# Optimization experiments

Measured on AMD Instinct MI355X. Metric: run time of the kernel, lower is better.

Reference implementation:

```python
import jax, jax.numpy as jnp
import numpy as np


def setup_inputs() -> dict:
    key = jax.random.key(0)
    k1, k2, k3, k4 = jax.random.split(key, 4)
    B, S, D_IN, D_OUT = 4, 4096, 768, 128
    x = jax.random.normal(k1, (B, S, D_IN), dtype=jnp.float32)
    # torch Linear(d_in, d_out) weight is [d_out, d_in]; we store transposed [d_in, d_out]
    scale = 1.0 / np.sqrt(D_IN)
    Wq = jax.random.normal(k2, (D_IN, D_OUT), dtype=jnp.float32) * scale
    Wk = jax.random.normal(k3, (D_IN, D_OUT), dtype=jnp.float32) * scale
    Wv = jax.random.normal(k4, (D_IN, D_OUT), dtype=jnp.float32) * scale
    return {"x": x, "Wq": Wq, "Wk": Wk, "Wv": Wv}


def reference(x, Wq, Wk, Wv):
    # x: [B, S, d_in]; Wq/Wk/Wv: [d_in, d_out]
    B, S, _ = x.shape
    q = jnp.einsum('bsd,de->bse', x, Wq)
    k = jnp.einsum('bsd,de->bse', x, Wk)
    v = jnp.einsum('bsd,de->bse', x, Wv)
    d_out = k.shape[-1]
    scores = jnp.einsum('bqe,bke->bqk', q, k)  # [B, S, S]
    causal = jnp.tril(jnp.ones((S, S), dtype=bool))  # True where attention allowed
    scores = jnp.where(causal[None], scores, -jnp.inf)
    attn = jax.nn.softmax(scores / jnp.sqrt(jnp.float32(d_out)), axis=-1)
    # dropout prob is 0.0 -> identity
    return jnp.einsum('bqk,bke->bqe', attn, v)
```

## Files before the change

kernel.cpp:

```cpp
#include <hip/hip_runtime.h>
#include <stdint.h>

typedef unsigned short u16;
typedef uint32_t u32;
typedef __bf16 bf16;
typedef bf16 bf16x8 __attribute__((ext_vector_type(8)));
typedef bf16 bf16x4 __attribute__((ext_vector_type(4)));
typedef short s16x4 __attribute__((ext_vector_type(4)));
typedef float f32x4 __attribute__((ext_vector_type(4)));
typedef uint32_t u32x4 __attribute__((ext_vector_type(4)));

#define S_LEN 4096
#define D_IN 768
#define D_OUT 128
#define NB 4
#define M_TOTAL (NB * S_LEN)
#define NPROP 115

__device__ const unsigned char SPLITS_T[16] = {1,2,3,4,4,5,6,7,8,8,9,10,11,12,12,13};
__device__ const unsigned char OFF_T[16]    = {0,1,3,6,10,14,19,25,32,40,48,57,67,78,90,102};
__device__ const unsigned char TILE_OF[NPROP] = {
    0, 1,1, 2,2,2, 3,3,3,3, 4,4,4,4, 5,5,5,5,5, 6,6,6,6,6,6, 7,7,7,7,7,7,7,
    8,8,8,8,8,8,8,8, 9,9,9,9,9,9,9,9, 10,10,10,10,10,10,10,10,10,
    11,11,11,11,11,11,11,11,11,11, 12,12,12,12,12,12,12,12,12,12,12,
    13,13,13,13,13,13,13,13,13,13,13,13, 14,14,14,14,14,14,14,14,14,14,14,14,
    15,15,15,15,15,15,15,15,15,15,15,15,15};

static __device__ __forceinline__ u16 f2bf(float f) {
    union { float f; uint32_t u; } c; c.f = f;
    return (u16)((c.u + 0x7FFFu + ((c.u >> 16) & 1u)) >> 16);
}
static __device__ __forceinline__ float bf2f_lo(uint32_t w) { return __uint_as_float(w << 16); }
static __device__ __forceinline__ float bf2f_hi(uint32_t w) { return __uint_as_float(w & 0xFFFF0000u); }

static __device__ __forceinline__ bf16x8 ld8(const u16* p) {
    union { u32x4 v; bf16x8 b; } c;
    c.v = *reinterpret_cast<const u32x4*>(p);
    return c.b;
}

static __device__ __forceinline__ f32x4 mfma16(bf16x8 a, bf16x8 b, f32x4 c) {
    return __builtin_amdgcn_mfma_f32_16x16x32_bf16(a, b, c, 0, 0, 0);
}

static __device__ __forceinline__ f32x4 mfma16k16(uint2 a, uint2 b, f32x4 c) {
#if defined(__HIP_DEVICE_COMPILE__)
#if __has_builtin(__builtin_amdgcn_mfma_f32_16x16x16_bf16)
    union { uint2 u; bf16x4 v; } ca, cb; ca.u = a; cb.u = b;
    return __builtin_amdgcn_mfma_f32_16x16x16_bf16(ca.v, cb.v, c, 0, 0, 0);
#else
    union { uint2 u; s16x4 v; } ca, cb; ca.u = a; cb.u = b;
    return __builtin_amdgcn_mfma_f32_16x16x16bf16_1k(ca.v, cb.v, c, 0, 0, 0);
#endif
#else
    (void)a; (void)b;
    return c;
#endif
}

static __device__ __forceinline__ void gload16(const void* g, void* l) {
    __builtin_amdgcn_global_load_lds((const __attribute__((address_space(1))) uint32_t*)g,
                                     (__attribute__((address_space(3))) uint32_t*)l, 16, 0, 0);
}

static __device__ __forceinline__ float bpermf(int addr, float v) {
    return __int_as_float(__builtin_amdgcn_ds_bpermute(addr, __float_as_int(v)));
}
static __device__ __forceinline__ u32 pk2(float a, float b) {
    return __builtin_amdgcn_perm(__float_as_uint(b), __float_as_uint(a), 0x07060302u);
}

__global__ __launch_bounds__(256) void wt_kernel(const float* __restrict__ Wq, const float* __restrict__ Wk,
                                                 const float* __restrict__ Wv, u16* __restrict__ Wt) {
    __shared__ u16 tl[128][40];
    const int w = blockIdx.x / 24;
    const int kc = (blockIdx.x % 24) * 32;
    const float* W = (w == 0) ? Wq : (w == 1) ? Wk : Wv;
#pragma unroll
    for (int p = 0; p < 4; ++p) {
        int kr = p * 8 + (threadIdx.x >> 5);
        int nc = (threadIdx.x & 31) * 4;
        float4 v = *reinterpret_cast<const float4*>(W + (size_t)(kc + kr) * D_OUT + nc);
        tl[nc + 0][kr] = f2bf(v.x); tl[nc + 1][kr] = f2bf(v.y);
        tl[nc + 2][kr] = f2bf(v.z); tl[nc + 3][kr] = f2bf(v.w);
    }
    __syncthreads();
    const int n = threadIdx.x >> 1, kh = (threadIdx.x & 1) * 16;
    u32x4* dst = reinterpret_cast<u32x4*>(Wt + (size_t)w * D_OUT * D_IN + (size_t)n * D_IN + kc + kh);
    const u32x4* src = reinterpret_cast<const u32x4*>(&tl[n][kh]);
    dst[0] = src[0];
    dst[1] = src[1];
}

__global__ __launch_bounds__(256) void qkv_kernel(const float* __restrict__ x, const u16* __restrict__ Wt,
                                                  u16* __restrict__ Qb, u16* __restrict__ Kb,
                                                  u16* __restrict__ Vt) {
    __shared__ __align__(16) u16 wslab[2][192 * 32];
    __shared__ __align__(16) float xslab[2][32 * 32];
    const int wave = threadIdx.x >> 6, lane = threadIdx.x & 63;
    const int r = lane & 15, g = lane >> 4;
    const int m0 = blockIdx.x * 32;
    const int h = blockIdx.y;

    f32x4 acc[3][2];
#pragma unroll
    for (int y = 0; y < 3; ++y)
#pragma unroll
        for (int f = 0; f < 2; ++f) acc[y][f] = f32x4{0.f, 0.f, 0.f, 0.f};

    auto stageW = [&](int bb, int kk) {
#pragma unroll
        for (int i = 0; i < 3; ++i) {
            int c = wave * 3 + i;
            int rr = c * 16 + (lane >> 2);
            int gr = (rr >> 6) * 128 + h * 64 + (rr & 63);
            const u16* src = Wt + (size_t)gr * D_IN + kk * 32 + (((lane & 3) ^ (rr & 3)) * 8);
            gload16(src, &wslab[bb][c * 512]);
        }
    };
    auto stageX = [&](int bb, int kk) {
        int c = wave;
        int row = c * 8 + (lane >> 3);
        const float* src = x + (size_t)(m0 + row) * D_IN + kk * 32 + (((lane & 7) ^ (row & 7)) * 4);
        gload16(src, &xslab[bb][c * 256]);
    };

    stageW(0, 0);
    stageX(0, 0);
    int buf = 0;
    const int arow = (wave >> 1) * 16 + r;
    const int ch = (wave & 1) * 32;
    for (int kk = 0; kk < 24; ++kk) {
        int kn = (kk + 1 < 24) ? kk + 1 : 0;
        stageX(buf ^ 1, kn);
        stageW(buf ^ 1, kn);
        asm volatile("s_waitcnt vmcnt(4)" ::: "memory");
        __builtin_amdgcn_sched_barrier(0);
        __builtin_amdgcn_s_barrier();
        f32x4 xa0 = *reinterpret_cast<const f32x4*>(&xslab[buf][arow * 32 + (((2 * g) ^ (arow & 7)) * 4)]);
        f32x4 xa1 = *reinterpret_cast<const f32x4*>(&xslab[buf][arow * 32 + (((2 * g + 1) ^ (arow & 7)) * 4)]);
        union { u16 u[8]; bf16x8 bv; } af;
#pragma unroll
        for (int t = 0; t < 4; ++t) { af.u[t] = f2bf(xa0[t]); af.u[4 + t] = f2bf(xa1[t]); }
#pragma unroll
        for (int y = 0; y < 3; ++y)
#pragma unroll
            for (int f = 0; f < 2; ++f) {
                int rr = y * 64 + ch + f * 16 + r;
                bf16x8 wf = ld8(&wslab[buf][rr * 32 + ((g ^ (r & 3)) * 8)]);
                acc[y][f] = mfma16(af.bv, wf, acc[y][f]);
            }
        __builtin_amdgcn_s_barrier();
        buf ^= 1;
    }
    asm volatile("s_waitcnt vmcnt(0)" ::: "memory");

    const float QSC = 0.1275174366f;
#pragma unroll
    for (int f = 0; f < 2; ++f)
#pragma unroll
        for (int i = 0; i < 4; ++i) {
            int mrow = m0 + (wave >> 1) * 16 + 4 * g + i;
            int col = h * 64 + ch + f * 16 + r;
            Qb[(size_t)mrow * D_OUT + col] = f2bf(acc[0][f][i] * QSC);
            Kb[(size_t)mrow * D_OUT + col] = f2bf(acc[1][f][i]);
            Vt[((size_t)((mrow >> 12) * D_OUT + col)) * S_LEN + (mrow & 4095)] = f2bf(acc[2][f][i]);
        }
}

__global__ __launch_bounds__(512, 2) void attn_kernel(const u16* __restrict__ Qb, const u16* __restrict__ Kb,
                                                      const u16* __restrict__ Vt, u16* __restrict__ Po,
                                                      float* __restrict__ Pml, float* __restrict__ out,
                                                      int mode) {
    __shared__ __align__(16) u16 kbuf[2][64 * 128];
    __shared__ __align__(16) u16 vbuf[2][128 * 64];

    const int wave = threadIdx.x >> 6, lane = threadIdx.x & 63;
    const int r = lane & 15, g = lane >> 4;
    const int n = (int)blockIdx.x;
    int b, t, s, sp;
    if (mode) {
        b = n / NPROP;
        const int idx = n - b * NPROP;
        t = TILE_OF[idx];
        s = idx - OFF_T[t];
        sp = SPLITS_T[t];
    } else {
        b = n >> 4; t = n & 15; s = 0; sp = 1;
    }
    const int nj = 4 * t + 4;
    const int qw0 = t * 256 + wave * 32;

    const u16* Kp = Kb + (size_t)b * S_LEN * D_OUT;
    const u16* Vp = Vt + (size_t)b * D_OUT * S_LEN;

    bf16x8 qf[2][4];
#pragma unroll
    for (int rb = 0; rb < 2; ++rb)
#pragma unroll
        for (int kk = 0; kk < 4; ++kk)
            qf[rb][kk] = ld8(Qb + ((size_t)(b * S_LEN + qw0 + rb * 16 + r)) * D_OUT + kk * 32 + 8 * g);

    f32x4 o[2][8];
    float l_[2];
#pragma unroll
    for (int rb = 0; rb < 2; ++rb) {
#pragma unroll
        for (int f = 0; f < 8; ++f) o[rb][f] = f32x4{0.f, 0.f, 0.f, 0.f};
        l_[rb] = 0.f;
    }

    const int lx16 = (lane ^ 16) * 4, lx32 = (lane ^ 32) * 4;

    auto stageK = [&](int bb, int k0) {
#pragma unroll
        for (int i = 0; i < 2; ++i) {
            int c = i * 8 + wave;
            int row = c * 4 + (lane >> 4);
            const u16* src = Kp + (size_t)(k0 + row) * D_OUT + (((lane & 15) ^ (row & 7)) * 8);
            gload16(src, &kbuf[bb][c * 512]);
        }
    };
    auto stageV = [&](int bb, int k0) {
#pragma unroll
        for (int i = 0; i < 2; ++i) {
            int c = i * 8 + wave;
            int row = c * 8 + (lane >> 3);
            const u16* src = Vp + (size_t)row * S_LEN + k0 + (((lane & 7) ^ (row & 7)) * 8);
            gload16(src, &vbuf[bb][c * 512]);
        }
    };

    stageK(0, s * 64);
    stageV(0, s * 64);
    int buf = 0;
    for (int j = s; j < nj; j += sp) {
        const int k0 = j * 64;
        asm volatile("s_waitcnt vmcnt(0)" ::: "memory");
        __builtin_amdgcn_sched_barrier(0);
        __builtin_amdgcn_s_barrier();
        const int j2 = j + sp;
        if (j2 < nj) {
            stageK(buf ^ 1, j2 * 64);
            stageV(buf ^ 1, j2 * 64);
        }

        f32x4 sv[2][4];
#pragma unroll
        for (int rb = 0; rb < 2; ++rb)
#pragma unroll
            for (int f = 0; f < 4; ++f) sv[rb][f] = f32x4{0.f, 0.f, 0.f, 0.f};
        __builtin_amdgcn_s_setprio(1);
#pragma unroll
        for (int kk = 0; kk < 4; ++kk)
#pragma unroll
            for (int f = 0; f < 4; ++f) {
                bf16x8 kf = ld8(&kbuf[buf][(f * 16 + r) * 128 + (((kk * 4 + g) ^ (r & 7)) * 8)]);
                sv[0][f] = mfma16(kf, qf[0][kk], sv[0][f]);
                sv[1][f] = mfma16(kf, qf[1][kk], sv[1][f]);
            }
        __builtin_amdgcn_s_setprio(0);

        uint2 pb[2][4];
#pragma unroll
        for (int rb = 0; rb < 2; ++rb) {
            const int qrb = qw0 + rb * 16;
            const int q = qrb + r;
            if (k0 + 63 > qrb) {
#pragma unroll
                for (int f = 0; f < 4; ++f)
#pragma unroll
                    for (int i = 0; i < 4; ++i)
                        if (k0 + 16 * f + 4 * g + i > q) sv[rb][f][i] = -1e30f;
            }
            float r0 = 0.f;
#pragma unroll
            for (int f = 0; f < 4; ++f)
#pragma unroll
                for (int i = 0; i < 4; ++i) {
                    float p = __builtin_amdgcn_exp2f(sv[rb][f][i]);
                    sv[rb][f][i] = p;
                    r0 += p;
                }
            l_[rb] += r0;
#pragma unroll
            for (int kb = 0; kb < 4; ++kb) {
                pb[rb][kb].x = pk2(sv[rb][kb][0], sv[rb][kb][1]);
                pb[rb][kb].y = pk2(sv[rb][kb][2], sv[rb][kb][3]);
            }
        }

        __builtin_amdgcn_s_setprio(1);
#pragma unroll
        for (int kb = 0; kb < 4; ++kb) {
            const int vs = ((2 * kb + (g >> 1)) ^ (r & 7)) * 8 + 4 * (g & 1);
#pragma unroll
            for (int f = 0; f < 8; ++f) {
                uint2 vf = *reinterpret_cast<const uint2*>(&vbuf[buf][(f * 16 + r) * 64 + vs]);
                o[0][f] = mfma16k16(vf, pb[0][kb], o[0][f]);
                o[1][f] = mfma16k16(vf, pb[1][kb], o[1][f]);
            }
        }
        __builtin_amdgcn_s_setprio(0);
        buf ^= 1;
    }
    asm volatile("s_waitcnt vmcnt(0)" ::: "memory");

    l_[0] += bpermf(lx16, l_[0]);
    l_[1] += bpermf(lx16, l_[1]);
    l_[0] += bpermf(lx32, l_[0]);
    l_[1] += bpermf(lx32, l_[1]);

    if (!mode) {
#pragma unroll
        for (int rb = 0; rb < 2; ++rb) {
            float inv = 1.0f / l_[rb];
            float* orow = out + ((size_t)(b * S_LEN + qw0 + rb * 16 + r)) * D_OUT;
#pragma unroll
            for (int f = 0; f < 8; ++f) {
                float4 v;
                v.x = o[rb][f][0] * inv; v.y = o[rb][f][1] * inv;
                v.z = o[rb][f][2] * inv; v.w = o[rb][f][3] * inv;
                *reinterpret_cast<float4*>(orow + 16 * f + 4 * g) = v;
            }
        }
    } else {
        u16* po = Po + (size_t)n * (256 * 128);
        float* pml = Pml + (size_t)n * 512;
#pragma unroll
        for (int rb = 0; rb < 2; ++rb) {
            u16* chunk0 = po + (size_t)((wave * 2 + rb) * 8) * 256 + lane * 4;
#pragma unroll
            for (int f = 0; f < 8; ++f) {
                u32 w0 = (u32)f2bf(o[rb][f][0]) | ((u32)f2bf(o[rb][f][1]) << 16);
                u32 w1 = (u32)f2bf(o[rb][f][2]) | ((u32)f2bf(o[rb][f][3]) << 16);
                uint2 ww; ww.x = w0; ww.y = w1;
                *reinterpret_cast<uint2*>(chunk0 + f * 256) = ww;
            }
            if (g == 0) {
                const int row = wave * 32 + rb * 16 + r;
                pml[row * 2 + 0] = 0.f;
                pml[row * 2 + 1] = l_[rb];
            }
        }
    }
}

__global__ __launch_bounds__(256) void merge_kernel(const u16* __restrict__ Po, const float* __restrict__ Pml,
                                                    float* __restrict__ out) {
    const int gr = blockIdx.x * 16 + (threadIdx.x >> 4);
    const int c0 = (threadIdx.x & 15) * 8;
    const int b = gr >> 12, rr = gr & 4095;
    const int t = rr >> 8, row = rr & 255;
    const int ns = SPLITS_T[t];
    const size_t pbase = (size_t)b * NPROP + OFF_T[t];

    const int wv = row >> 5, rbm = (row >> 4) & 1, r_ = row & 15;
    const int fm = c0 >> 4, g0 = (c0 >> 2) & 3;
    const size_t coff = (size_t)((wv * 2 + rbm) * 8 + fm) * 256;

    float L = 0.f;
    for (int s = 0; s < ns; ++s) L += Pml[(pbase + s) * 512 + row * 2 + 1];
    const float inv = 1.0f / L;

    float acc[8];
#pragma unroll
    for (int k = 0; k < 8; ++k) acc[k] = 0.f;
    for (int s = 0; s < ns; ++s) {
        const u16* chunk = Po + (pbase + s) * (256 * 128) + coff;
        uint2 pv0 = *reinterpret_cast<const uint2*>(chunk + (g0 * 16 + r_) * 4);
        uint2 pv1 = *reinterpret_cast<const uint2*>(chunk + ((g0 + 1) * 16 + r_) * 4);
        acc[0] += bf2f_lo(pv0.x); acc[1] += bf2f_hi(pv0.x);
        acc[2] += bf2f_lo(pv0.y); acc[3] += bf2f_hi(pv0.y);
        acc[4] += bf2f_lo(pv1.x); acc[5] += bf2f_hi(pv1.x);
        acc[6] += bf2f_lo(pv1.y); acc[7] += bf2f_hi(pv1.y);
    }
    float* op = out + (size_t)gr * D_OUT + c0;
    float4 v0, v1;
    v0.x = acc[0] * inv; v0.y = acc[1] * inv; v0.z = acc[2] * inv; v0.w = acc[3] * inv;
    v1.x = acc[4] * inv; v1.y = acc[5] * inv; v1.z = acc[6] * inv; v1.w = acc[7] * inv;
    *reinterpret_cast<float4*>(op) = v0;
    *reinterpret_cast<float4*>(op + 4) = v1;
}

extern "C" void kernel_launch(void* const* d_in, const int* in_sizes, int n_in,
                              void* d_out, int out_size, void* d_ws, size_t ws_size,
                              hipStream_t stream) {
    const float* x  = (const float*)d_in[0];
    const float* Wq = (const float*)d_in[1];
    const float* Wk = (const float*)d_in[2];
    const float* Wv = (const float*)d_in[3];
    float* out = (float*)d_out;

    u16* Qb = (u16*)d_ws;
    u16* Kb = Qb + (size_t)M_TOTAL * D_OUT;
    u16* Vt = Kb + (size_t)M_TOTAL * D_OUT;
    u16* Wt = Vt + (size_t)M_TOTAL * D_OUT;

    const unsigned long long base = (3ULL * M_TOTAL * D_OUT + 3ULL * D_OUT * D_IN) * 2ULL;
    const unsigned long long perP = 256ULL * 128 * 2 + 512ULL * 4;
    const int nblk = NPROP * NB;
    const int mode = (ws_size >= base + (unsigned long long)nblk * perP) ? 1 : 0;

    u16* Po = Wt + (size_t)3 * D_OUT * D_IN;
    float* Pml = (float*)(Po + (size_t)nblk * (256 * 128));

    wt_kernel<<<72, 256, 0, stream>>>(Wq, Wk, Wv, Wt);
    qkv_kernel<<<dim3(512, 2), 256, 0, stream>>>(x, Wt, Qb, Kb, Vt);
    attn_kernel<<<mode ? nblk : 16 * NB, 512, 0, stream>>>(Qb, Kb, Vt, Po, Pml, out, mode);
    if (mode)
        merge_kernel<<<M_TOTAL / 16, 256, 0, stream>>>(Po, Pml, out);
}
```

Baseline: 94.84 us.

## Restructure QKV projection: one weight per block, weights read directly from global

The QKV projection kernel changes its tiling. Each block now computes a 64-row by 128-column output for one of Q, K or V (grid 256x3) instead of 32 rows by 64 columns across all three (grid 512x2). Weight fragments are loaded straight from global memory (relying on cache) instead of being staged in LDS, and only x is double-buffered in LDS, in 64-wide k chunks. The aim is to cut LDS traffic and sync overhead per MFMA, at the cost of x being read three times and uncoalesced per-lane weight loads from global.

```diff
diff --git a/kernel.cpp b/kernel.cpp
--- a/kernel.cpp
+++ b/kernel.cpp
@@ -95,77 +95,81 @@
 __global__ __launch_bounds__(256) void qkv_kernel(const float* __restrict__ x, const u16* __restrict__ Wt,
                                                   u16* __restrict__ Qb, u16* __restrict__ Kb,
                                                   u16* __restrict__ Vt) {
-    __shared__ __align__(16) u16 wslab[2][192 * 32];
-    __shared__ __align__(16) float xslab[2][32 * 32];
+    __shared__ __align__(16) float xslab[2][64 * 64];
     const int wave = threadIdx.x >> 6, lane = threadIdx.x & 63;
     const int r = lane & 15, g = lane >> 4;
-    const int m0 = blockIdx.x * 32;
-    const int h = blockIdx.y;
-
-    f32x4 acc[3][2];
-#pragma unroll
-    for (int y = 0; y < 3; ++y)
-#pragma unroll
-        for (int f = 0; f < 2; ++f) acc[y][f] = f32x4{0.f, 0.f, 0.f, 0.f};
-
-    auto stageW = [&](int bb, int kk) {
-#pragma unroll
-        for (int i = 0; i < 3; ++i) {
-            int c = wave * 3 + i;
-            int rr = c * 16 + (lane >> 2);
-            int gr = (rr >> 6) * 128 + h * 64 + (rr & 63);
-            const u16* src = Wt + (size_t)gr * D_IN + kk * 32 + (((lane & 3) ^ (rr & 3)) * 8);
-            gload16(src, &wslab[bb][c * 512]);
+    const int m0 = blockIdx.x * 64;
+    const int y = blockIdx.y;
+    const u16* wt = Wt + (size_t)y * D_OUT * D_IN;
+
+    f32x4 acc[8];
+#pragma unroll
+    for (int f = 0; f < 8; ++f) acc[f] = f32x4{0.f, 0.f, 0.f, 0.f};
+
+    auto stageX = [&](int bb, int kk) {
+#pragma unroll
+        for (int i = 0; i < 4; ++i) {
+            int c = wave * 4 + i;
+            int row = c * 4 + (lane >> 4);
+            int slot = (lane & 15) ^ (row & 7);
+            const float* src = x + (size_t)(m0 + row) * D_IN + kk * 64 + slot * 4;
+            gload16(src, &xslab[bb][c * 256]);
         }
     };
-    auto stageX = [&](int bb, int kk) {
-        int c = wave;
-        int row = c * 8 + (lane >> 3);
-        const float* src = x + (size_t)(m0 + row) * D_IN + kk * 32 + (((lane & 7) ^ (row & 7)) * 4);
-        gload16(src, &xslab[bb][c * 256]);
-    };
-
-    stageW(0, 0);
+
     stageX(0, 0);
     int buf = 0;
-    const int arow = (wave >> 1) * 16 + r;
-    const int ch = (wave & 1) * 32;
-    for (int kk = 0; kk < 24; ++kk) {
-        int kn = (kk + 1 < 24) ? kk + 1 : 0;
-        stageX(buf ^ 1, kn);
-        stageW(buf ^ 1, kn);
-        asm volatile("s_waitcnt vmcnt(4)" ::: "memory");
+    const int arow = wave * 16 + r;
+    for (int kk = 0; kk < 12; ++kk) {
+        asm volatile("s_waitcnt vmcnt(0)" ::: "memory");
         __builtin_amdgcn_sched_barrier(0);
         __builtin_amdgcn_s_barrier();
-        f32x4 xa0 = *reinterpret_cast<const f32x4*>(&xslab[buf][arow * 32 + (((2 * g) ^ (arow & 7)) * 4)]);
-        f32x4 xa1 = *reinterpret_cast<const f32x4*>(&xslab[buf][arow * 32 + (((2 * g + 1) ^ (arow & 7)) * 4)]);
-        union { u16 u[8]; bf16x8 bv; } af;
-#pragma unroll
-        for (int t = 0; t < 4; ++t) { af.u[t] = f2bf(xa0[t]); af.u[4 + t] = f2bf(xa1[t]); }
-#pragma unroll
-        for (int y = 0; y < 3; ++y)
-#pragma unroll
-            for (int f = 0; f < 2; ++f) {
-                int rr = y * 64 + ch + f * 16 + r;
-                bf16x8 wf = ld8(&wslab[buf][rr * 32 + ((g ^ (r & 3)) * 8)]);
-                acc[y][f] = mfma16(af.bv, wf, acc[y][f]);
-            }
-        __builtin_amdgcn_s_barrier();
+        if (kk + 1 < 12) stageX(buf ^ 1, kk + 1);
+#pragma unroll
+        for (int kk2 = 0; kk2 < 2; ++kk2) {
+            f32x4 xa0 = *reinterpret_cast<const f32x4*>(
+                &xslab[buf][arow * 64 + (((kk2 * 8 + 2 * g) ^ (arow & 7)) * 4)]);
+            f32x4 xa1 = *reinterpret_cast<const f32x4*>(
+                &xslab[buf][arow * 64 + (((kk2 * 8 + 2 * g + 1) ^ (arow & 7)) * 4)]);
+            union { u16 u[8]; bf16x8 bv; } af;
+#pragma unroll
+            for (int t = 0; t < 4; ++t) { af.u[t] = f2bf(xa0[t]); af.u[4 + t] = f2bf(xa1[t]); }
+#pragma unroll
+            for (int f = 0; f < 8; ++f) {
+                bf16x8 wf = ld8(wt + (size_t)(f * 16 + r) * D_IN + kk * 64 + kk2 * 32 + 8 * g);
+                acc[f] = mfma16(af.bv, wf, acc[f]);
+            }
+        }
         buf ^= 1;
     }
     asm volatile("s_waitcnt vmcnt(0)" ::: "memory");
 
     const float QSC = 0.1275174366f;
-#pragma unroll
-    for (int f = 0; f < 2; ++f)
-#pragma unroll
-        for (int i = 0; i < 4; ++i) {
-            int mrow = m0 + (wave >> 1) * 16 + 4 * g + i;
-            int col = h * 64 + ch + f * 16 + r;
-            Qb[(size_t)mrow * D_OUT + col] = f2bf(acc[0][f][i] * QSC);
-            Kb[(size_t)mrow * D_OUT + col] = f2bf(acc[1][f][i]);
-            Vt[((size_t)((mrow >> 12) * D_OUT + col)) * S_LEN + (mrow & 4095)] = f2bf(acc[2][f][i]);
-        }
+    if (y == 0) {
+#pragma unroll
+        for (int f = 0; f < 8; ++f)
+#pragma unroll
+            for (int i = 0; i < 4; ++i) {
+                int mrow = m0 + wave * 16 + 4 * g + i;
+                Qb[(size_t)mrow * D_OUT + f * 16 + r] = f2bf(acc[f][i] * QSC);
+            }
+    } else if (y == 1) {
+#pragma unroll
+        for (int f = 0; f < 8; ++f)
+#pragma unroll
+            for (int i = 0; i < 4; ++i) {
+                int mrow = m0 + wave * 16 + 4 * g + i;
+                Kb[(size_t)mrow * D_OUT + f * 16 + r] = f2bf(acc[f][i]);
+            }
+    } else {
+#pragma unroll
+        for (int f = 0; f < 8; ++f)
+#pragma unroll
+            for (int i = 0; i < 4; ++i) {
+                int mrow = m0 + wave * 16 + 4 * g + i;
+                Vt[((size_t)((mrow >> 12) * D_OUT + f * 16 + r)) * S_LEN + (mrow & 4095)] = f2bf(acc[f][i]);
+            }
+    }
 }
 
 __global__ __launch_bounds__(512, 2) void attn_kernel(const u16* __restrict__ Qb, const u16* __restrict__ Kb,
@@ -406,7 +410,7 @@
     float* Pml = (float*)(Po + (size_t)nblk * (256 * 128));
 
     wt_kernel<<<72, 256, 0, stream>>>(Wq, Wk, Wv, Wt);
-    qkv_kernel<<<dim3(512, 2), 256, 0, stream>>>(x, Wt, Qb, Kb, Vt);
+    qkv_kernel<<<dim3(256, 3), 256, 0, stream>>>(x, Wt, Qb, Kb, Vt);
     attn_kernel<<<mode ? nblk : 16 * NB, 512, 0, stream>>>(Qb, Kb, Vt, Po, Pml, out, mode);
     if (mode)
         merge_kernel<<<M_TOTAL / 16, 256, 0, stream>>>(Po, Pml, out);
```

Result: slower. 135.4 us (+42.8%).
